# Performance work log

Hardware: AMD Instinct MI355X
Metric: run time of the kernel (lower is better)

## Reference

```python
import jax, jax.numpy as jnp
import numpy as np

P = 10      # qubits
LQ = 4      # re-uploading layers
B = 4096    # batch
HID = 32    # readout hidden
DIM = 2 ** P


def _rz(t):
    t = jnp.asarray(t, jnp.float32)
    e = jnp.exp(-0.5j * t.astype(jnp.complex64))
    z = jnp.zeros_like(e)
    return jnp.stack([jnp.stack([e, z], -1), jnp.stack([z, jnp.conj(e)], -1)], -2)


def _rx(t):
    t = jnp.asarray(t, jnp.float32)
    c = jnp.cos(0.5 * t).astype(jnp.complex64)
    s = jnp.sin(0.5 * t).astype(jnp.complex64)
    return jnp.stack([jnp.stack([c, -1j * s], -1), jnp.stack([-1j * s, c], -1)], -2)


def _ry(t):
    t = jnp.asarray(t, jnp.float32)
    c = jnp.cos(0.5 * t).astype(jnp.complex64)
    s = jnp.sin(0.5 * t).astype(jnp.complex64)
    return jnp.stack([jnp.stack([c, -s], -1), jnp.stack([s, c], -1)], -2)


def _apply_1q(state, U, k):
    # state [B, 2^P] complex, U [B,2,2]; wire 0 = most-significant bit (PennyLane order)
    b = state.shape[0]
    s = state.reshape(b, 2 ** k, 2, -1)
    s = jnp.einsum('bij,bajc->baic', U, s)
    return s.reshape(b, -1)


def _apply_cnot(state, c, t):
    b = state.shape[0]
    a, d = min(c, t), max(c, t)
    s = state.reshape(b, 2 ** a, 2, 2 ** (d - a - 1), 2, -1)
    if c == a:  # control = smaller wire index (axis 2), target at axis 4
        hi = jnp.flip(s[:, :, 1], axis=3)  # [b,pre,mid,2,post] -> flip target bit
        s = jnp.stack([s[:, :, 0], hi], axis=2)
    else:       # control = larger wire index (axis 4), target at axis 2
        hi = jnp.flip(s[:, :, :, :, 1], axis=2)  # [b,pre,2,mid,post] -> flip target bit
        s = jnp.stack([s[:, :, :, :, 0], hi], axis=4)
    return s.reshape(b, -1)


def _meas_signs(p):
    # rows 0..p-1: Z_k signs; rows p..2p-1: Z_k Z_{(k+1)%p} signs
    idx = np.arange(2 ** p)
    bits = (idx[None, :] >> (p - 1 - np.arange(p)[:, None])) & 1
    z = (1.0 - 2.0 * bits).astype(np.float32)            # [p, 2^p]
    zz = z * np.roll(z, -1, axis=0)                      # [p, 2^p]
    return jnp.asarray(np.concatenate([z, zz], axis=0))  # [2p, 2^p]


MEAS = _meas_signs(P)


def _circuit_feats(theta, rot_weights, enc_scale, enc_bias):
    b = theta.shape[0]
    # Hadamard on every wire of |0...0> -> uniform superposition
    state = jnp.full((b, DIM), 1.0 / np.sqrt(DIM), dtype=jnp.complex64)
    for l in range(LQ):
        for k in range(P):
            t0 = enc_scale[l, k, 0] * theta[:, k] + enc_bias[l, k, 0]
            t1 = enc_scale[l, k, 1] * theta[:, k] + enc_bias[l, k, 1]
            U_enc = jnp.einsum('bij,bjk->bik', _rx(t1), _rz(t0))  # RX(t1) RZ(t0)
            w = rot_weights[l, k]
            # PennyLane Rot(phi,theta,omega) = RZ(omega) RY(theta) RZ(phi)
            U_rot = _rz(w[2]) @ _ry(w[1]) @ _rz(w[0])
            U = jnp.einsum('ij,bjk->bik', U_rot, U_enc)
            state = _apply_1q(state, U, k)
        for k in range(P):
            state = _apply_cnot(state, k, (k + 1) % P)
    probs = jnp.abs(state) ** 2              # [B, 2^P]
    return probs @ MEAS.T                    # [B, 2P] expectation values


def setup_inputs() -> dict:
    key = jax.random.key(0)
    ks = jax.random.split(key, 4)
    theta = jax.random.uniform(ks[0], (B, P), jnp.float32, -np.pi, np.pi)
    rot_weights = 0.02 * jax.random.normal(ks[1], (LQ, P, 3), dtype=jnp.float32)
    enc_scale = jnp.ones((LQ, P, 2), jnp.float32)   # clamp(0.5,1.5) of ones = ones
    enc_bias = jnp.zeros((LQ, P, 2), jnp.float32)
    n_meas = 2 * P
    W1 = jax.random.normal(ks[2], (HID, n_meas), dtype=jnp.float32) / np.sqrt(n_meas)
    b1 = jnp.zeros((HID,), jnp.float32)
    W2 = jax.random.normal(ks[3], (1, HID), dtype=jnp.float32) / np.sqrt(HID)
    b2 = jnp.zeros((1,), jnp.float32)
    return dict(theta=theta, rot_weights=rot_weights, enc_scale=enc_scale,
                enc_bias=enc_bias, W1=W1, b1=b1, W2=W2, b2=b2)


def reference(theta, rot_weights, enc_scale, enc_bias, W1, b1, W2, b2):
    feats = _circuit_feats(theta, rot_weights, enc_scale, enc_bias)
    h = jax.nn.silu(feats @ W1.T + b1)
    return (h @ W2.T + b2)[:, 0]  # [B]
```

## Files before the change

kernel.cpp:

```cpp
#include <hip/hip_runtime.h>
#include <math.h>

#define NQ   10
#define NLAY 4
#define BATCH 4096
#define HID  32
#define NM   20

typedef float    f2  __attribute__((ext_vector_type(2)));
typedef unsigned u2v __attribute__((ext_vector_type(2)));

struct Tables {
    unsigned col[NLAY + 1][NQ];
    unsigned row[NLAY + 1][NQ];
};

constexpr Tables make_tables() {
    Tables t{};
    unsigned col[NQ] = {}, row[NQ] = {};
    for (int k = 0; k < NQ; ++k) { col[k] = 1u << (NQ - 1 - k); row[k] = 1u << (NQ - 1 - k); }
    for (int l = 0; l <= NLAY; ++l) {
        for (int k = 0; k < NQ; ++k) { t.col[l][k] = col[k]; t.row[l][k] = row[k]; }
        for (int k = 0; k < NQ; ++k) {
            int c = k, tg = (k + 1) % NQ;
            col[c] ^= col[tg];
            row[tg] ^= row[c];
        }
    }
    return t;
}

static constexpr Tables TB = make_tables();

struct cpx { float x, y; };
__device__ __forceinline__ cpx cxmul(cpx a, cpx b) {
    return { fmaf(a.x, b.x, -a.y * b.y), fmaf(a.x, b.y, a.y * b.x) };
}

__device__ __forceinline__ f2 mk2(float a, float b) { f2 r; r[0] = a; r[1] = b; return r; }
__device__ __forceinline__ f2 ffma(f2 a, f2 b, f2 c) { return __builtin_elementwise_fma(a, b, c); }

__device__ __forceinline__ f2 cmac(f2 acc, f2 a, f2 b) {
    acc = ffma(mk2(a[0], a[0]), b, acc);
    acc = ffma(mk2(-a[1], a[1]), mk2(b[1], b[0]), acc);
    return acc;
}

template<int CTRL>
__device__ __forceinline__ float dppf(float x) {
    return __int_as_float(__builtin_amdgcn_update_dpp(
        0, __float_as_int(x), CTRL, 0xF, 0xF, true));
}

template<unsigned M>
__device__ __forceinline__ float dpplo(float x) {
    static_assert(M < 16u, "dpplo handles masks 0..15");
    if constexpr (M == 0u)       return x;
    else if constexpr (M == 1u)  return dppf<0xB1>(x);
    else if constexpr (M == 2u)  return dppf<0x4E>(x);
    else if constexpr (M == 3u)  return dppf<0x1B>(x);
    else if constexpr (M == 7u)  return dppf<0x141>(x);
    else if constexpr (M == 8u)  return dppf<0x128>(x);
    else if constexpr (M == 15u) return dppf<0x140>(x);
    else if constexpr (M == 4u)  return dppf<0x141>(dppf<0x1B>(x));
    else if constexpr (M == 5u)  return dppf<0x141>(dppf<0x4E>(x));
    else if constexpr (M == 6u)  return dppf<0x141>(dppf<0xB1>(x));
    else if constexpr (M == 9u)  return dppf<0x128>(dppf<0xB1>(x));
    else if constexpr (M == 10u) return dppf<0x128>(dppf<0x4E>(x));
    else if constexpr (M == 11u) return dppf<0x128>(dppf<0x1B>(x));
    else if constexpr (M == 12u) return dppf<0x140>(dppf<0x1B>(x));
    else if constexpr (M == 13u) return dppf<0x140>(dppf<0x4E>(x));
    else                         return dppf<0x140>(dppf<0xB1>(x));
}

__device__ __forceinline__ float redfold16(float x) {
#if __has_builtin(__builtin_amdgcn_permlane16_swap)
    u2v r = __builtin_amdgcn_permlane16_swap(__float_as_uint(x), __float_as_uint(x), false, false);
    return __uint_as_float(r[0]) + __uint_as_float(r[1]);
#else
    return x + __shfl_xor(x, 16);
#endif
}

__device__ __forceinline__ float redfold32(float x) {
#if __has_builtin(__builtin_amdgcn_permlane32_swap)
    u2v r = __builtin_amdgcn_permlane32_swap(__float_as_uint(x), __float_as_uint(x), false, false);
    return __uint_as_float(r[0]) + __uint_as_float(r[1]);
#else
    return x + __shfl_xor(x, 32);
#endif
}

template<unsigned M>
__device__ __forceinline__ float xlane(float x) {
    if constexpr (M == 0u) return x;
    else if constexpr ((M & 32u) != 0u)
        return __shfl_xor(x, (int)M);
    else if constexpr ((M & 16u) != 0u)
        return __int_as_float(__builtin_amdgcn_ds_swizzle(
            __float_as_int(x), (int)((M << 10) | 0x1F)));
    else return dpplo<M>(x);
}

template<int L, int K>
__device__ __forceinline__ void apply_gate(f2 (&st)[16], const float4 (*gm)[2],
                                           const int lane) {
    constexpr unsigned v     = TB.col[L][K];
    constexpr unsigned m     = TB.row[L][K];
    constexpr unsigned vlane = (v >> 4) & 63u;
    constexpr int      vr    = (int)(v & 15u);
    constexpr unsigned mlane = (m >> 4) & 63u;
    constexpr int      mr    = (int)(m & 15u);
    constexpr int      gi    = L * NQ + K;

    int laneP = 0;
    if constexpr (mlane != 0u) laneP = __popc((unsigned)lane & mlane) & 1;
    const float4 A = gm[gi][laneP];
    const f2 ocA = mk2(A.x, A.y), pcA = mk2(A.z, A.w);
    f2 ocB = ocA, pcB = pcA;
    if constexpr (mr != 0) {
        const float4 B = gm[gi][laneP ^ 1];
        ocB = mk2(B.x, B.y); pcB = mk2(B.z, B.w);
    }

    #pragma unroll
    for (int r = 0; r < 16; ++r) {
        const int r2 = r ^ vr;
        if (r2 < r) continue;
        f2 p_r, p_r2;
        if constexpr (vlane != 0u) {
            p_r = mk2(xlane<vlane>(st[r2][0]), xlane<vlane>(st[r2][1]));
            if (r2 != r)
                p_r2 = mk2(xlane<vlane>(st[r][0]), xlane<vlane>(st[r][1]));
        } else {
            p_r = st[r2];
            p_r2 = st[r];
        }
        {
            const int pr = __builtin_popcount((unsigned)(r & mr)) & 1;
            const f2 oc = pr ? ocB : ocA;
            const f2 pc = pr ? pcB : pcA;
            f2 acc = mk2(0.f, 0.f);
            acc = cmac(acc, oc, st[r]);
            acc = cmac(acc, pc, p_r);
            if (r2 != r) {
                const int pr2 = __builtin_popcount((unsigned)(r2 & mr)) & 1;
                const f2 oc2 = pr2 ? ocB : ocA;
                const f2 pc2 = pr2 ? pcB : pcA;
                f2 acc2 = mk2(0.f, 0.f);
                acc2 = cmac(acc2, oc2, st[r2]);
                acc2 = cmac(acc2, pc2, p_r2);
                st[r2] = acc2;
            }
            st[r] = acc;
        }
    }
}

__global__ __launch_bounds__(256, 4)
void qrh_kernel(
    const float* __restrict__ theta, const float* __restrict__ rotw,
    const float* __restrict__ escale, const float* __restrict__ ebias,
    const float* __restrict__ W1, const float* __restrict__ b1,
    const float* __restrict__ W2, const float* __restrict__ b2,
    float* __restrict__ out)
{
    __shared__ float4 gmat[4 * NLAY * NQ][2];
    __shared__ float4 wtab[4][NQ];

    const int tid  = threadIdx.x;
    const int lane = tid & 63;
    const int wv   = tid >> 6;
    const int e    = wv;
    const int b    = blockIdx.x * 4 + e;

    for (int g = tid; g < 4 * NLAY * NQ; g += 256) {
        const int ge = g / (NLAY * NQ);
        const int gg = g % (NLAY * NQ);
        const int l = gg / NQ, k = gg % NQ;
        const int gb = blockIdx.x * 4 + ge;
        const float th = theta[gb * NQ + k];
        const int e2 = (l * NQ + k) * 2;
        const float t0 = escale[e2 + 0] * th + ebias[e2 + 0];
        const float t1 = escale[e2 + 1] * th + ebias[e2 + 1];
        float sn0, c0, sn1, c1;
        __sincosf(0.5f * t0, &sn0, &c0);
        __sincosf(0.5f * t1, &sn1, &c1);
        const f2 E00 = mk2( c1 * c0,  -c1 * sn0);
        const f2 E01 = mk2( sn1 * sn0, -sn1 * c0);
        const f2 E10 = mk2(-sn1 * sn0, -sn1 * c0);
        const f2 E11 = mk2( c1 * c0,   c1 * sn0);
        const int r3 = (l * NQ + k) * 3;
        const float w0 = rotw[r3 + 0], w1 = rotw[r3 + 1], w2 = rotw[r3 + 2];
        float cw, sw, ca0, sa0, ca1, sa1;
        __sincosf(0.5f * w1, &sw, &cw);
        __sincosf(0.5f * (w0 + w2), &sa0, &ca0);
        __sincosf(0.5f * (w0 - w2), &sa1, &ca1);
        const f2 R00 = mk2( cw * ca0, -cw * sa0);
        const f2 R01 = mk2(-sw * ca1, -sw * sa1);
        const f2 R10 = mk2( sw * ca1, -sw * sa1);
        const f2 R11 = mk2( cw * ca0,  cw * sa0);
        auto cm = [](f2 a, f2 bb) { return mk2(a[0]*bb[0] - a[1]*bb[1], a[0]*bb[1] + a[1]*bb[0]); };
        const f2 U00 = cm(R00, E00) + cm(R01, E10);
        const f2 U01 = cm(R00, E01) + cm(R01, E11);
        const f2 U10 = cm(R10, E00) + cm(R11, E10);
        const f2 U11 = cm(R10, E01) + cm(R11, E11);
        gmat[g][0] = make_float4(U00[0], U00[1], U01[0], U01[1]);
        gmat[g][1] = make_float4(U11[0], U11[1], U10[0], U10[1]);
        if (l == 0) {
            const float inv = 0.70710678118654752f;
            const f2 al = (U00 + U01) * inv;
            const f2 be = (U10 + U11) * inv;
            wtab[ge][k] = make_float4(al[0], al[1], be[0], be[1]);
        }
    }
    __syncthreads();

    if (wv & 1) { __builtin_amdgcn_s_sleep(10); __builtin_amdgcn_s_sleep(10); }

    f2 st[16];
    {
        cpx pre;
        {
            const float4 q = wtab[e][0];
            pre = ((lane >> 5) & 1) ? cpx{q.z, q.w} : cpx{q.x, q.y};
            #pragma unroll
            for (int k = 1; k < 6; ++k) {
                const float4 t = wtab[e][k];
                const cpx w_ = ((lane >> (5 - k)) & 1) ? cpx{t.z, t.w} : cpx{t.x, t.y};
                pre = cxmul(pre, w_);
            }
        }
        const float4 q6 = wtab[e][6], q7 = wtab[e][7];
        const float4 q8 = wtab[e][8], q9 = wtab[e][9];
        const cpx w6[2] = {{q6.x, q6.y}, {q6.z, q6.w}};
        const cpx w7[2] = {{q7.x, q7.y}, {q7.z, q7.w}};
        const cpx w8[2] = {{q8.x, q8.y}, {q8.z, q8.w}};
        const cpx w9[2] = {{q9.x, q9.y}, {q9.z, q9.w}};
        cpx a67[4];
        #pragma unroll
        for (int j = 0; j < 4; ++j)
            a67[j] = cxmul(cxmul(pre, w6[j >> 1]), w7[j & 1]);
        cpx w89[4];
        #pragma unroll
        for (int j = 0; j < 4; ++j)
            w89[j] = cxmul(w8[j >> 1], w9[j & 1]);
        #pragma unroll
        for (int r = 0; r < 16; ++r) {
            const cpx t = cxmul(a67[r >> 2], w89[r & 3]);
            st[r] = mk2(t.x, t.y);
        }
    }

    const float4 (*gm)[2] = &gmat[e * NLAY * NQ];

    #define GATE(L,K) apply_gate<L,K>(st, gm, lane);
    #define LAYER(L) GATE(L,0) GATE(L,1) GATE(L,2) GATE(L,3) GATE(L,4) \
                     GATE(L,5) GATE(L,6) GATE(L,7) GATE(L,8) GATE(L,9)
    LAYER(1)
    LAYER(2)
    LAYER(3)
    #undef LAYER
    #undef GATE

    float w[16];
    #pragma unroll
    for (int r = 0; r < 16; ++r) {
        const f2 sq = st[r] * st[r];
        w[r] = sq[0] + sq[1];
    }
    #pragma unroll
    for (int bit = 1; bit < 16; bit <<= 1) {
        #pragma unroll
        for (int j = 0; j < 16; ++j) {
            if (!(j & bit)) {
                const float a = w[j], c = w[j | bit];
                w[j] = a + c; w[j | bit] = a - c;
            }
        }
    }

    float feats[NM];
    #pragma unroll
    for (int f = 0; f < NM; ++f) {
        const unsigned M = (f < NQ) ? TB.row[NLAY][f]
                                    : (TB.row[NLAY][f - NQ] ^ TB.row[NLAY][(f - NQ + 1) % NQ]);
        const unsigned Mlane = (M >> 4) & 63u;
        const int Mr = (int)(M & 15u);
        const float s = w[Mr];
        const int lsgn = __popc((unsigned)lane & Mlane) & 1;
        feats[f] = lsgn ? -s : s;
    }
    #pragma unroll
    for (int f = 0; f < NM; ++f) {
        float v = feats[f];
        v += dppf<0xB1>(v);
        v += dppf<0x4E>(v);
        v += dppf<0x141>(v);
        v += dppf<0x128>(v);
        v = redfold16(v);
        v = redfold32(v);
        feats[f] = v;
    }

    const int hl = lane & 31;
    float part;
    {
        float acc = b1[hl];
        #pragma unroll
        for (int mm = 0; mm < NM; ++mm) acc = fmaf(feats[mm], W1[hl * NM + mm], acc);
        const float sg = 1.f / (1.f + __expf(-acc));
        part = acc * sg * W2[hl];
    }
    part += dppf<0xB1>(part);
    part += dppf<0x4E>(part);
    part += dppf<0x141>(part);
    part += dppf<0x128>(part);
    part = redfold16(part);
    part = redfold32(part);
    if (lane == 0) out[b] = fmaf(0.5f, part, b2[0]);
}

extern "C" void kernel_launch(void* const* d_in, const int* in_sizes, int n_in,
                              void* d_out, int out_size, void* d_ws, size_t ws_size,
                              hipStream_t stream) {
    (void)in_sizes; (void)n_in; (void)out_size; (void)d_ws; (void)ws_size;
    const float* theta = (const float*)d_in[0];
    const float* rotw  = (const float*)d_in[1];
    const float* esc   = (const float*)d_in[2];
    const float* ebi   = (const float*)d_in[3];
    const float* W1    = (const float*)d_in[4];
    const float* b1    = (const float*)d_in[5];
    const float* W2    = (const float*)d_in[6];
    const float* b2    = (const float*)d_in[7];
    float* out = (float*)d_out;

    qrh_kernel<<<BATCH / 4, 256, 0, stream>>>(theta, rotw, esc, ebi, W1, b1, W2, b2, out);
}
```

Before: 97.08 us.

## Split each batch state vector across two wavefronts with LDS exchange

Each batch element's 1024-amplitude state now spans two wavefronts of 64 lanes with 8 amplitudes per lane, instead of one wavefront holding 16 per lane. Gates on the top qubit bit exchange amplitudes through shared memory with block barriers, and the measurement features are summed across the two waves via LDS. This cuts registers per thread and raises the number of waves in flight, at the cost of extra syncthreads, LDS traffic and 4x more blocks.

```diff
diff --git a/kernel.cpp b/kernel.cpp
--- a/kernel.cpp
+++ b/kernel.cpp
@@ -103,18 +103,22 @@
 }
 
 template<int L, int K>
-__device__ __forceinline__ void apply_gate(f2 (&st)[16], const float4 (*gm)[2],
-                                           const int lane) {
+__device__ __forceinline__ void apply_gate(f2 (&st)[8], const float4 (*gm)[2],
+                                           const int lane, const int wv,
+                                           const int tid, f2 (*xch)[128]) {
     constexpr unsigned v     = TB.col[L][K];
     constexpr unsigned m     = TB.row[L][K];
-    constexpr unsigned vlane = (v >> 4) & 63u;
-    constexpr int      vr    = (int)(v & 15u);
-    constexpr unsigned mlane = (m >> 4) & 63u;
-    constexpr int      mr    = (int)(m & 15u);
+    constexpr unsigned vw    = (v >> 9) & 1u;
+    constexpr unsigned vlane = (v >> 3) & 63u;
+    constexpr int      vr    = (int)(v & 7u);
+    constexpr unsigned mw    = (m >> 9) & 1u;
+    constexpr unsigned mlane = (m >> 3) & 63u;
+    constexpr int      mr    = (int)(m & 7u);
     constexpr int      gi    = L * NQ + K;
 
     int laneP = 0;
     if constexpr (mlane != 0u) laneP = __popc((unsigned)lane & mlane) & 1;
+    if constexpr (mw != 0u)    laneP ^= (wv & 1);
     const float4 A = gm[gi][laneP];
     const f2 ocA = mk2(A.x, A.y), pcA = mk2(A.z, A.w);
     f2 ocB = ocA, pcB = pcA;
@@ -123,8 +127,28 @@
         ocB = mk2(B.x, B.y); pcB = mk2(B.z, B.w);
     }
 
-    #pragma unroll
-    for (int r = 0; r < 16; ++r) {
+    if constexpr (vw != 0u) {
+        __syncthreads();
+        #pragma unroll
+        for (int r = 0; r < 8; ++r) xch[r][tid] = st[r];
+        __syncthreads();
+        const int ptid = tid ^ (64 | (int)vlane);
+        #pragma unroll
+        for (int r = 0; r < 8; ++r) {
+            const f2 po = xch[r ^ vr][ptid];
+            const int pr = __builtin_popcount((unsigned)(r & mr)) & 1;
+            const f2 oc = pr ? ocB : ocA;
+            const f2 pc = pr ? pcB : pcA;
+            f2 acc = mk2(0.f, 0.f);
+            acc = cmac(acc, oc, st[r]);
+            acc = cmac(acc, pc, po);
+            st[r] = acc;
+        }
+        return;
+    }
+
+    #pragma unroll
+    for (int r = 0; r < 8; ++r) {
         const int r2 = r ^ vr;
         if (r2 < r) continue;
         f2 p_r, p_r2;
@@ -157,7 +181,7 @@
     }
 }
 
-__global__ __launch_bounds__(256, 4)
+__global__ __launch_bounds__(128, 8)
 void qrh_kernel(
     const float* __restrict__ theta, const float* __restrict__ rotw,
     const float* __restrict__ escale, const float* __restrict__ ebias,
@@ -165,21 +189,19 @@
     const float* __restrict__ W2, const float* __restrict__ b2,
     float* __restrict__ out)
 {
-    __shared__ float4 gmat[4 * NLAY * NQ][2];
-    __shared__ float4 wtab[4][NQ];
+    __shared__ float4 gmat[NLAY * NQ][2];
+    __shared__ float4 wtab[NQ];
+    __shared__ f2     xch[8][128];
+    __shared__ float  fbuf[2][NM];
 
     const int tid  = threadIdx.x;
     const int lane = tid & 63;
     const int wv   = tid >> 6;
-    const int e    = wv;
-    const int b    = blockIdx.x * 4 + e;
-
-    for (int g = tid; g < 4 * NLAY * NQ; g += 256) {
-        const int ge = g / (NLAY * NQ);
-        const int gg = g % (NLAY * NQ);
-        const int l = gg / NQ, k = gg % NQ;
-        const int gb = blockIdx.x * 4 + ge;
-        const float th = theta[gb * NQ + k];
+    const int b    = blockIdx.x;
+
+    if (tid < NLAY * NQ) {
+        const int l = tid / NQ, k = tid % NQ;
+        const float th = theta[b * NQ + k];
         const int e2 = (l * NQ + k) * 2;
         const float t0 = escale[e2 + 0] * th + ebias[e2 + 0];
         const float t1 = escale[e2 + 1] * th + ebias[e2 + 1];
@@ -205,56 +227,46 @@
         const f2 U01 = cm(R00, E01) + cm(R01, E11);
         const f2 U10 = cm(R10, E00) + cm(R11, E10);
         const f2 U11 = cm(R10, E01) + cm(R11, E11);
-        gmat[g][0] = make_float4(U00[0], U00[1], U01[0], U01[1]);
-        gmat[g][1] = make_float4(U11[0], U11[1], U10[0], U10[1]);
+        gmat[tid][0] = make_float4(U00[0], U00[1], U01[0], U01[1]);
+        gmat[tid][1] = make_float4(U11[0], U11[1], U10[0], U10[1]);
         if (l == 0) {
             const float inv = 0.70710678118654752f;
             const f2 al = (U00 + U01) * inv;
             const f2 be = (U10 + U11) * inv;
-            wtab[ge][k] = make_float4(al[0], al[1], be[0], be[1]);
+            wtab[k] = make_float4(al[0], al[1], be[0], be[1]);
         }
     }
     __syncthreads();
 
-    if (wv & 1) { __builtin_amdgcn_s_sleep(10); __builtin_amdgcn_s_sleep(10); }
-
-    f2 st[16];
+    f2 st[8];
     {
         cpx pre;
         {
-            const float4 q = wtab[e][0];
-            pre = ((lane >> 5) & 1) ? cpx{q.z, q.w} : cpx{q.x, q.y};
+            const float4 q = wtab[0];
+            pre = wv ? cpx{q.z, q.w} : cpx{q.x, q.y};
             #pragma unroll
-            for (int k = 1; k < 6; ++k) {
-                const float4 t = wtab[e][k];
-                const cpx w_ = ((lane >> (5 - k)) & 1) ? cpx{t.z, t.w} : cpx{t.x, t.y};
+            for (int k = 1; k < 7; ++k) {
+                const float4 t = wtab[k];
+                const cpx w_ = ((lane >> (6 - k)) & 1) ? cpx{t.z, t.w} : cpx{t.x, t.y};
                 pre = cxmul(pre, w_);
             }
         }
-        const float4 q6 = wtab[e][6], q7 = wtab[e][7];
-        const float4 q8 = wtab[e][8], q9 = wtab[e][9];
-        const cpx w6[2] = {{q6.x, q6.y}, {q6.z, q6.w}};
+        const float4 q7 = wtab[7], q8 = wtab[8], q9 = wtab[9];
         const cpx w7[2] = {{q7.x, q7.y}, {q7.z, q7.w}};
         const cpx w8[2] = {{q8.x, q8.y}, {q8.z, q8.w}};
         const cpx w9[2] = {{q9.x, q9.y}, {q9.z, q9.w}};
-        cpx a67[4];
-        #pragma unroll
-        for (int j = 0; j < 4; ++j)
-            a67[j] = cxmul(cxmul(pre, w6[j >> 1]), w7[j & 1]);
         cpx w89[4];
         #pragma unroll
         for (int j = 0; j < 4; ++j)
             w89[j] = cxmul(w8[j >> 1], w9[j & 1]);
         #pragma unroll
-        for (int r = 0; r < 16; ++r) {
-            const cpx t = cxmul(a67[r >> 2], w89[r & 3]);
+        for (int r = 0; r < 8; ++r) {
+            const cpx t = cxmul(cxmul(pre, w7[r >> 2]), w89[r & 3]);
             st[r] = mk2(t.x, t.y);
         }
     }
 
-    const float4 (*gm)[2] = &gmat[e * NLAY * NQ];
-
-    #define GATE(L,K) apply_gate<L,K>(st, gm, lane);
+    #define GATE(L,K) apply_gate<L,K>(st, gmat, lane, wv, tid, xch);
     #define LAYER(L) GATE(L,0) GATE(L,1) GATE(L,2) GATE(L,3) GATE(L,4) \
                      GATE(L,5) GATE(L,6) GATE(L,7) GATE(L,8) GATE(L,9)
     LAYER(1)
@@ -263,16 +275,16 @@
     #undef LAYER
     #undef GATE
 
-    float w[16];
-    #pragma unroll
-    for (int r = 0; r < 16; ++r) {
+    float w[8];
+    #pragma unroll
+    for (int r = 0; r < 8; ++r) {
         const f2 sq = st[r] * st[r];
         w[r] = sq[0] + sq[1];
     }
     #pragma unroll
-    for (int bit = 1; bit < 16; bit <<= 1) {
-        #pragma unroll
-        for (int j = 0; j < 16; ++j) {
+    for (int bit = 1; bit < 8; bit <<= 1) {
+        #pragma unroll
+        for (int j = 0; j < 8; ++j) {
             if (!(j & bit)) {
                 const float a = w[j], c = w[j | bit];
                 w[j] = a + c; w[j | bit] = a - c;
@@ -285,10 +297,11 @@
     for (int f = 0; f < NM; ++f) {
         const unsigned M = (f < NQ) ? TB.row[NLAY][f]
                                     : (TB.row[NLAY][f - NQ] ^ TB.row[NLAY][(f - NQ + 1) % NQ]);
-        const unsigned Mlane = (M >> 4) & 63u;
-        const int Mr = (int)(M & 15u);
+        const unsigned Mw    = (M >> 9) & 1u;
+        const unsigned Mlane = (M >> 3) & 63u;
+        const int Mr = (int)(M & 7u);
         const float s = w[Mr];
-        const int lsgn = __popc((unsigned)lane & Mlane) & 1;
+        const int lsgn = (__popc((unsigned)lane & Mlane) ^ (Mw & (unsigned)wv)) & 1;
         feats[f] = lsgn ? -s : s;
     }
     #pragma unroll
@@ -302,6 +315,14 @@
         v = redfold32(v);
         feats[f] = v;
     }
+    __syncthreads();
+    #pragma unroll
+    for (int f = 0; f < NM; ++f)
+        if (lane == f) fbuf[wv][f] = feats[f];
+    __syncthreads();
+    #pragma unroll
+    for (int f = 0; f < NM; ++f)
+        feats[f] = fbuf[0][f] + fbuf[1][f];
 
     const int hl = lane & 31;
     float part;
@@ -318,7 +339,7 @@
     part += dppf<0x128>(part);
     part = redfold16(part);
     part = redfold32(part);
-    if (lane == 0) out[b] = fmaf(0.5f, part, b2[0]);
+    if (tid == 0) out[b] = fmaf(0.5f, part, b2[0]);
 }
 
 extern "C" void kernel_launch(void* const* d_in, const int* in_sizes, int n_in,
@@ -335,5 +356,5 @@
     const float* b2    = (const float*)d_in[7];
     float* out = (float*)d_out;
 
-    qrh_kernel<<<BATCH / 4, 256, 0, stream>>>(theta, rotw, esc, ebi, W1, b1, W2, b2, out);
-}
+    qrh_kernel<<<BATCH, 128, 0, stream>>>(theta, rotw, esc, ebi, W1, b1, W2, b2, out);
+}
```

New measurement: 99.62 us. 2.6% more time.
